# Kernel optimization log

Hardware: AMD Instinct MI355X
Metric: run time of the kernel (lower is better)

Reference implementation:

```python
import jax, jax.numpy as jnp
import numpy as np

N_NODES = 100000
N_EDGES = 1000000

def _gcn_conv(x, W, b, src, dst, n_nodes):
    # PyG GCNConv: linear first, then symmetric-normalized aggregation with self loops
    x = x @ W  # [N, F_out]
    loop = jnp.arange(n_nodes, dtype=src.dtype)
    src2 = jnp.concatenate([src, loop])
    dst2 = jnp.concatenate([dst, loop])
    deg = jax.ops.segment_sum(jnp.ones(src2.shape[0], x.dtype), dst2, num_segments=n_nodes)
    dinv = jnp.where(deg > 0, jax.lax.rsqrt(deg), 0.0)
    norm = dinv[src2] * dinv[dst2]  # [E+N]
    msgs = x[src2] * norm[:, None]  # gather + scale
    out = jax.ops.segment_sum(msgs, dst2, num_segments=n_nodes)  # scatter-add
    return out + b

def _pair_norm_si(x):
    # mode 'PN-SI', scale=1
    x = x - x.mean(axis=0)
    row_norm = jnp.sqrt(1e-6 + jnp.sum(x * x, axis=1, keepdims=True))
    return x / row_norm

def setup_inputs() -> dict:
    key = jax.random.key(0)
    k1, k2, k3, k4 = jax.random.split(key, 4)
    in_c, hid_c, out_c = 256, 64, 40
    x = jax.random.normal(k1, (N_NODES, in_c), dtype=jnp.float32)
    edge_index = jax.random.randint(k2, (2, N_EDGES), 0, N_NODES, dtype=jnp.int64)
    W1 = jax.random.normal(k3, (in_c, hid_c), dtype=jnp.float32) / np.sqrt(in_c)
    b1 = jnp.zeros((hid_c,), jnp.float32)
    W2 = jax.random.normal(k4, (hid_c, out_c), dtype=jnp.float32) / np.sqrt(hid_c)
    b2 = jnp.zeros((out_c,), jnp.float32)
    return {"x": x, "edge_index": edge_index, "W1": W1, "b1": b1, "W2": W2, "b2": b2}

def reference(x, edge_index, W1, b1, W2, b2):
    src, dst = edge_index[0], edge_index[1]
    n = x.shape[0]
    h = jax.nn.relu(_gcn_conv(x, W1, b1, src, dst, n))
    h = _gcn_conv(h, W2, b2, src, dst, n)
    h = _pair_norm_si(h)
    return jax.nn.log_softmax(h, axis=1)
```

## Files before the change

### kernel.cpp

```cpp
#include <hip/hip_runtime.h>
#include <hip/hip_fp16.h>
#include <math.h>

#define F_IN  256
#define F_HID 64
#define F_OUT 40
#define HS2_LD 64

__global__ void k_deg(const int* __restrict__ dst, unsigned* __restrict__ degc, int E) {
    int i = blockIdx.x * blockDim.x + threadIdx.x;
    if (i < E) atomicAdd(&degc[dst[i]], 1u);
}

__global__ __launch_bounds__(256) void k_scanA(const unsigned* __restrict__ degc,
                                               unsigned* __restrict__ exscan,
                                               unsigned* __restrict__ bsum, int N) {
    __shared__ unsigned s[256];
    int tid = threadIdx.x;
    int i = blockIdx.x * 256 + tid;
    unsigned v = (i < N) ? degc[i] : 0u;
    s[tid] = v;
    __syncthreads();
    for (int off = 1; off < 256; off <<= 1) {
        unsigned t = (tid >= off) ? s[tid - off] : 0u;
        __syncthreads();
        s[tid] += t;
        __syncthreads();
    }
    if (i < N) exscan[i] = s[tid] - v;
    if (tid == 255) bsum[blockIdx.x] = s[255];
}

__global__ __launch_bounds__(512) void k_scanB(unsigned* __restrict__ bsum, int nb) {
    __shared__ unsigned s[512];
    int tid = threadIdx.x;
    unsigned v = (tid < nb) ? bsum[tid] : 0u;
    s[tid] = v;
    __syncthreads();
    for (int off = 1; off < 512; off <<= 1) {
        unsigned t = (tid >= off) ? s[tid - off] : 0u;
        __syncthreads();
        s[tid] += t;
        __syncthreads();
    }
    if (tid < nb) bsum[tid] = s[tid] - v;
}

__global__ void k_scanC(const unsigned* __restrict__ degc, const unsigned* __restrict__ exscan,
                        const unsigned* __restrict__ bsum, unsigned* __restrict__ rowptr,
                        float* __restrict__ dinv, int N, int E) {
    int i = blockIdx.x * blockDim.x + threadIdx.x;
    if (i < N) {
        rowptr[i] = exscan[i] + bsum[i >> 8];
        dinv[i] = rsqrtf((float)degc[i] + 1.0f);
        if (i == 0) rowptr[N] = (unsigned)E;
    }
}

__global__ void k_fill(const int* __restrict__ src, const int* __restrict__ dst,
                       const unsigned* __restrict__ rowptr, unsigned* __restrict__ cursor,
                       unsigned* __restrict__ col, int E) {
    int e = blockIdx.x * blockDim.x + threadIdx.x;
    if (e >= E) return;
    int d = dst[e];
    unsigned p = atomicAdd(&cursor[d], 1u);
    col[rowptr[d] + p] = (unsigned)src[e];
}

#define MM1_KC 32
#define MM1_XP 68
__global__ __launch_bounds__(256) void k_mm1(const float* __restrict__ x,
                                             const float* __restrict__ W1,
                                             const float* __restrict__ dinv,
                                             __half* __restrict__ hs1, int N) {
    __shared__ float sX[MM1_KC][MM1_XP];
    __shared__ float sW[MM1_KC][F_HID];
    int tid = threadIdx.x;
    int nbase = blockIdx.x * 64;
    int n0 = (tid & 15) * 4;
    int f0 = (tid >> 4) * 4;

    float acc[4][4];
    #pragma unroll
    for (int i = 0; i < 4; ++i)
        #pragma unroll
        for (int j = 0; j < 4; ++j) acc[i][j] = 0.f;

    for (int k0 = 0; k0 < F_IN; k0 += MM1_KC) {
        #pragma unroll
        for (int q = tid; q < 512; q += 256) {
            int row = q >> 3;
            int c4  = q & 7;
            int node = nbase + row;
            float4 v = (node < N) ? *(const float4*)(x + (size_t)node * F_IN + k0 + c4 * 4)
                                  : make_float4(0.f, 0.f, 0.f, 0.f);
            sX[c4 * 4 + 0][row] = v.x;
            sX[c4 * 4 + 1][row] = v.y;
            sX[c4 * 4 + 2][row] = v.z;
            sX[c4 * 4 + 3][row] = v.w;
        }
        #pragma unroll
        for (int q = tid; q < 512; q += 256) {
            int r  = q >> 4;
            int c4 = q & 15;
            *(float4*)&sW[r][c4 * 4] = *(const float4*)(W1 + (size_t)(k0 + r) * F_HID + c4 * 4);
        }
        __syncthreads();

        #pragma unroll
        for (int k = 0; k < MM1_KC; ++k) {
            float4 xv = *(const float4*)&sX[k][n0];
            float4 wv = *(const float4*)&sW[k][f0];
            acc[0][0] = fmaf(xv.x, wv.x, acc[0][0]); acc[0][1] = fmaf(xv.x, wv.y, acc[0][1]);
            acc[0][2] = fmaf(xv.x, wv.z, acc[0][2]); acc[0][3] = fmaf(xv.x, wv.w, acc[0][3]);
            acc[1][0] = fmaf(xv.y, wv.x, acc[1][0]); acc[1][1] = fmaf(xv.y, wv.y, acc[1][1]);
            acc[1][2] = fmaf(xv.y, wv.z, acc[1][2]); acc[1][3] = fmaf(xv.y, wv.w, acc[1][3]);
            acc[2][0] = fmaf(xv.z, wv.x, acc[2][0]); acc[2][1] = fmaf(xv.z, wv.y, acc[2][1]);
            acc[2][2] = fmaf(xv.z, wv.z, acc[2][2]); acc[2][3] = fmaf(xv.z, wv.w, acc[2][3]);
            acc[3][0] = fmaf(xv.w, wv.x, acc[3][0]); acc[3][1] = fmaf(xv.w, wv.y, acc[3][1]);
            acc[3][2] = fmaf(xv.w, wv.z, acc[3][2]); acc[3][3] = fmaf(xv.w, wv.w, acc[3][3]);
        }
        __syncthreads();
    }

    #pragma unroll
    for (int i = 0; i < 4; ++i) {
        int node = nbase + n0 + i;
        if (node < N) {
            float din = dinv[node];
            __half2* p = (__half2*)(hs1 + (size_t)node * F_HID + f0);
            p[0] = __floats2half2_rn(acc[i][0] * din, acc[i][1] * din);
            p[1] = __floats2half2_rn(acc[i][2] * din, acc[i][3] * din);
        }
    }
}

__global__ __launch_bounds__(256) void k_agg1(const unsigned* __restrict__ rowptr,
                                              const unsigned* __restrict__ col,
                                              const float* __restrict__ dinv,
                                              const __half* __restrict__ hs1,
                                              const float* __restrict__ bias1,
                                              float* __restrict__ agg1, int N) {
    int lane = threadIdx.x & 63;
    int w = blockIdx.x * 4 + (threadIdx.x >> 6);
    int na = 2 * w, nb = 2 * w + 1;
    if (na >= N) return;

    float dinA = dinv[na];
    unsigned aE = rowptr[na], aEnd = rowptr[na + 1];
    float accA = __half2float(hs1[(size_t)na * F_HID + lane]);

    bool hasB = (nb < N);
    float dinB = 0.f, accB = 0.f;
    unsigned bE = 0, bEnd = 0;
    if (hasB) {
        dinB = dinv[nb];
        bE = rowptr[nb]; bEnd = rowptr[nb + 1];
        accB = __half2float(hs1[(size_t)nb * F_HID + lane]);
    }

    while (aE + 4 <= aEnd && bE + 4 <= bEnd) {
        unsigned sa0 = col[aE], sa1 = col[aE + 1], sa2 = col[aE + 2], sa3 = col[aE + 3];
        unsigned sb0 = col[bE], sb1 = col[bE + 1], sb2 = col[bE + 2], sb3 = col[bE + 3];
        float va0 = __half2float(hs1[(size_t)sa0 * F_HID + lane]);
        float va1 = __half2float(hs1[(size_t)sa1 * F_HID + lane]);
        float va2 = __half2float(hs1[(size_t)sa2 * F_HID + lane]);
        float va3 = __half2float(hs1[(size_t)sa3 * F_HID + lane]);
        float vb0 = __half2float(hs1[(size_t)sb0 * F_HID + lane]);
        float vb1 = __half2float(hs1[(size_t)sb1 * F_HID + lane]);
        float vb2 = __half2float(hs1[(size_t)sb2 * F_HID + lane]);
        float vb3 = __half2float(hs1[(size_t)sb3 * F_HID + lane]);
        accA += (va0 + va1) + (va2 + va3);
        accB += (vb0 + vb1) + (vb2 + vb3);
        aE += 4; bE += 4;
    }
    while (aE + 4 <= aEnd) {
        unsigned s0 = col[aE], s1 = col[aE + 1], s2 = col[aE + 2], s3 = col[aE + 3];
        float v0 = __half2float(hs1[(size_t)s0 * F_HID + lane]);
        float v1 = __half2float(hs1[(size_t)s1 * F_HID + lane]);
        float v2 = __half2float(hs1[(size_t)s2 * F_HID + lane]);
        float v3 = __half2float(hs1[(size_t)s3 * F_HID + lane]);
        accA += (v0 + v1) + (v2 + v3);
        aE += 4;
    }
    while (bE + 4 <= bEnd) {
        unsigned s0 = col[bE], s1 = col[bE + 1], s2 = col[bE + 2], s3 = col[bE + 3];
        float v0 = __half2float(hs1[(size_t)s0 * F_HID + lane]);
        float v1 = __half2float(hs1[(size_t)s1 * F_HID + lane]);
        float v2 = __half2float(hs1[(size_t)s2 * F_HID + lane]);
        float v3 = __half2float(hs1[(size_t)s3 * F_HID + lane]);
        accB += (v0 + v1) + (v2 + v3);
        bE += 4;
    }
    while (aE < aEnd && bE < bEnd) {
        unsigned sa = col[aE], sb = col[bE];
        accA += __half2float(hs1[(size_t)sa * F_HID + lane]);
        accB += __half2float(hs1[(size_t)sb * F_HID + lane]);
        ++aE; ++bE;
    }
    while (aE < aEnd) { accA += __half2float(hs1[(size_t)col[aE] * F_HID + lane]); ++aE; }
    while (bE < bEnd) { accB += __half2float(hs1[(size_t)col[bE] * F_HID + lane]); ++bE; }

    float bv = bias1[lane];
    float vA = accA * dinA + bv;
    agg1[(size_t)na * F_HID + lane] = vA > 0.f ? vA : 0.f;
    if (hasB) {
        float vB = accB * dinB + bv;
        agg1[(size_t)nb * F_HID + lane] = vB > 0.f ? vB : 0.f;
    }
}

__global__ __launch_bounds__(320) void k_mm2(const float* __restrict__ a,
                                             const float* __restrict__ W2,
                                             const float* __restrict__ dinv,
                                             __half* __restrict__ hs2, int N) {
    __shared__ float sW[F_HID * F_OUT];
    int tid = threadIdx.x;
    for (int idx = tid; idx < F_HID * F_OUT; idx += 320) sW[idx] = W2[idx];
    __syncthreads();

    int f = tid % F_OUT, r = tid / F_OUT;
    int node = blockIdx.x * 8 + r;
    if (node >= N) return;
    const float* ar = a + (size_t)node * F_HID;
    float acc = 0.f;
    #pragma unroll 8
    for (int k = 0; k < F_HID; ++k) acc = fmaf(ar[k], sW[k * F_OUT + f], acc);
    hs2[(size_t)node * HS2_LD + f] = __float2half(acc * dinv[node]);
}

__global__ __launch_bounds__(256) void k_agg2(const unsigned* __restrict__ rowptr,
                                              const unsigned* __restrict__ col,
                                              const float* __restrict__ dinv,
                                              const __half* __restrict__ hs2,
                                              float* __restrict__ out,
                                              float* __restrict__ colsum, int N) {
    __shared__ float part[256];
    int lane = threadIdx.x & 63;
    int wid = threadIdx.x >> 6;
    int nwaves = gridDim.x * 4;
    float cacc = 0.f;
    if (lane < F_OUT) {
        for (int w = blockIdx.x * 4 + wid; 2 * w < N; w += nwaves) {
            int na = 2 * w, nb = 2 * w + 1;
            float dinA = dinv[na];
            unsigned aE = rowptr[na], aEnd = rowptr[na + 1];
            float accA = __half2float(hs2[(size_t)na * HS2_LD + lane]);
            bool hasB = (nb < N);
            float dinB = 0.f, accB = 0.f;
            unsigned bE = 0, bEnd = 0;
            if (hasB) {
                dinB = dinv[nb];
                bE = rowptr[nb]; bEnd = rowptr[nb + 1];
                accB = __half2float(hs2[(size_t)nb * HS2_LD + lane]);
            }

            while (aE + 4 <= aEnd && bE + 4 <= bEnd) {
                unsigned sa0 = col[aE], sa1 = col[aE + 1], sa2 = col[aE + 2], sa3 = col[aE + 3];
                unsigned sb0 = col[bE], sb1 = col[bE + 1], sb2 = col[bE + 2], sb3 = col[bE + 3];
                float va0 = __half2float(hs2[(size_t)sa0 * HS2_LD + lane]);
                float va1 = __half2float(hs2[(size_t)sa1 * HS2_LD + lane]);
                float va2 = __half2float(hs2[(size_t)sa2 * HS2_LD + lane]);
                float va3 = __half2float(hs2[(size_t)sa3 * HS2_LD + lane]);
                float vb0 = __half2float(hs2[(size_t)sb0 * HS2_LD + lane]);
                float vb1 = __half2float(hs2[(size_t)sb1 * HS2_LD + lane]);
                float vb2 = __half2float(hs2[(size_t)sb2 * HS2_LD + lane]);
                float vb3 = __half2float(hs2[(size_t)sb3 * HS2_LD + lane]);
                accA += (va0 + va1) + (va2 + va3);
                accB += (vb0 + vb1) + (vb2 + vb3);
                aE += 4; bE += 4;
            }
            while (aE + 4 <= aEnd) {
                unsigned s0 = col[aE], s1 = col[aE + 1], s2 = col[aE + 2], s3 = col[aE + 3];
                float v0 = __half2float(hs2[(size_t)s0 * HS2_LD + lane]);
                float v1 = __half2float(hs2[(size_t)s1 * HS2_LD + lane]);
                float v2 = __half2float(hs2[(size_t)s2 * HS2_LD + lane]);
                float v3 = __half2float(hs2[(size_t)s3 * HS2_LD + lane]);
                accA += (v0 + v1) + (v2 + v3);
                aE += 4;
            }
            while (bE + 4 <= bEnd) {
                unsigned s0 = col[bE], s1 = col[bE + 1], s2 = col[bE + 2], s3 = col[bE + 3];
                float v0 = __half2float(hs2[(size_t)s0 * HS2_LD + lane]);
                float v1 = __half2float(hs2[(size_t)s1 * HS2_LD + lane]);
                float v2 = __half2float(hs2[(size_t)s2 * HS2_LD + lane]);
                float v3 = __half2float(hs2[(size_t)s3 * HS2_LD + lane]);
                accB += (v0 + v1) + (v2 + v3);
                bE += 4;
            }
            while (aE < aEnd && bE < bEnd) {
                unsigned sa = col[aE], sb = col[bE];
                accA += __half2float(hs2[(size_t)sa * HS2_LD + lane]);
                accB += __half2float(hs2[(size_t)sb * HS2_LD + lane]);
                ++aE; ++bE;
            }
            while (aE < aEnd) { accA += __half2float(hs2[(size_t)col[aE] * HS2_LD + lane]); ++aE; }
            while (bE < bEnd) { accB += __half2float(hs2[(size_t)col[bE] * HS2_LD + lane]); ++bE; }

            accA *= dinA;
            out[(size_t)na * F_OUT + lane] = accA;
            cacc += accA;
            if (hasB) {
                accB *= dinB;
                out[(size_t)nb * F_OUT + lane] = accB;
                cacc += accB;
            }
        }
    }
    part[threadIdx.x] = cacc;
    __syncthreads();
    if (threadIdx.x < F_OUT) {
        float s = part[threadIdx.x] + part[64 + threadIdx.x] + part[128 + threadIdx.x] + part[192 + threadIdx.x];
        atomicAdd(&colsum[threadIdx.x], s);
    }
}

__global__ __launch_bounds__(128) void k_final(float* __restrict__ out,
                                               const float* __restrict__ colsum, int N) {
    __shared__ float sMean[F_OUT];
    if (threadIdx.x < F_OUT) sMean[threadIdx.x] = colsum[threadIdx.x] * (1.0f / (float)N);
    __syncthreads();
    int n = blockIdx.x * blockDim.x + threadIdx.x;
    if (n >= N) return;
    float* row = out + (size_t)n * F_OUT;
    float v[F_OUT];
    float ss = 0.f;
    #pragma unroll
    for (int f = 0; f < F_OUT; ++f) {
        float t = row[f] - sMean[f];
        v[f] = t;
        ss += t * t;
    }
    float scale = 1.0f / sqrtf(ss + 1e-6f);
    float m = -1e30f;
    #pragma unroll
    for (int f = 0; f < F_OUT; ++f) {
        float y = v[f] * scale;
        v[f] = y;
        m = fmaxf(m, y);
    }
    float sum = 0.f;
    #pragma unroll
    for (int f = 0; f < F_OUT; ++f) sum += expf(v[f] - m);
    float lse = logf(sum);
    #pragma unroll
    for (int f = 0; f < F_OUT; ++f) row[f] = v[f] - m - lse;
}

extern "C" void kernel_launch(void* const* d_in, const int* in_sizes, int n_in,
                              void* d_out, int out_size, void* d_ws, size_t ws_size,
                              hipStream_t stream) {
    const float* x  = (const float*)d_in[0];
    const int*   ei = (const int*)d_in[1];
    const float* W1 = (const float*)d_in[2];
    const float* b1 = (const float*)d_in[3];
    const float* W2 = (const float*)d_in[4];
    float* out = (float*)d_out;

    int N = in_sizes[0] / F_IN;
    int E = in_sizes[1] / 2;
    const int* src = ei;
    const int* dst = ei + E;

    unsigned* degc   = (unsigned*)d_ws;
    unsigned* cursor = degc + N;
    float*    colsum = (float*)(cursor + N);
    unsigned* rowptr = (unsigned*)(colsum + 64);
    unsigned* col    = rowptr + N + 1;
    float*    dinv   = (float*)(col + E);
    float*    agg1   = dinv + N;
    __half*   hs1    = (__half*)(agg1 + (size_t)64 * N);
    __half*   hs2    = hs1 + (size_t)64 * N;
    unsigned* exscan = (unsigned*)agg1;
    unsigned* bsum   = exscan + N;

    hipMemsetAsync(d_ws, 0, ((size_t)2 * N + 64) * sizeof(float), stream);

    int nA = (N + 255) / 256;
    k_deg<<<(E + 255) / 256, 256, 0, stream>>>(dst, degc, E);
    k_scanA<<<nA, 256, 0, stream>>>(degc, exscan, bsum, N);
    k_scanB<<<1, 512, 0, stream>>>(bsum, nA);
    k_scanC<<<nA, 256, 0, stream>>>(degc, exscan, bsum, rowptr, dinv, N, E);
    k_fill<<<(E + 255) / 256, 256, 0, stream>>>(src, dst, rowptr, cursor, col, E);
    k_mm1<<<(N + 63) / 64, 256, 0, stream>>>(x, W1, dinv, hs1, N);
    int waves1 = (N + 1) / 2;
    k_agg1<<<(waves1 + 3) / 4, 256, 0, stream>>>(rowptr, col, dinv, hs1, b1, agg1, N);
    k_mm2<<<(N + 7) / 8, 320, 0, stream>>>(agg1, W2, dinv, hs2, N);
    k_agg2<<<2048, 256, 0, stream>>>(rowptr, col, dinv, hs2, out, colsum, N);
    k_final<<<(N + 127) / 128, 128, 0, stream>>>(out, colsum, N);
}
```

Baseline: 448.6 us.

## Use fp16 MFMA for first-layer matmul with pre-transposed fp16 weights

Replaces the scalar FP32 FMA tiling in the first linear layer with 16x16x32 fp16 MFMA instructions. A small new kernel first converts W1 to a transposed fp16 copy, and each wave keeps its slice of that copy in registers. x tiles are converted to fp16 in shared memory, cutting compute time for the 100k x 256 x 64 matmul. The cost is fp16 rounding of the inputs, an extra kernel launch, and 2-byte scattered output stores in place of half2 stores.

```diff
diff --git a/kernel.cpp b/kernel.cpp
--- a/kernel.cpp
+++ b/kernel.cpp
@@ -6,6 +6,10 @@
 #define F_HID 64
 #define F_OUT 40
 #define HS2_LD 64
+
+typedef _Float16 h8 __attribute__((ext_vector_type(8)));
+typedef _Float16 h4 __attribute__((ext_vector_type(4)));
+typedef float f4 __attribute__((ext_vector_type(4)));
 
 __global__ void k_deg(const int* __restrict__ dst, unsigned* __restrict__ degc, int E) {
     int i = blockIdx.x * blockDim.x + threadIdx.x;
@@ -67,70 +71,70 @@
     col[rowptr[d] + p] = (unsigned)src[e];
 }
 
-#define MM1_KC 32
-#define MM1_XP 68
+__global__ void k_wt(const float* __restrict__ W1, __half* __restrict__ Wt) {
+    int i = blockIdx.x * 256 + threadIdx.x;
+    int k = i >> 6, n = i & 63;
+    Wt[n * 256 + k] = __float2half(W1[i]);
+}
+
+#define XS 136
 __global__ __launch_bounds__(256) void k_mm1(const float* __restrict__ x,
-                                             const float* __restrict__ W1,
+                                             const __half* __restrict__ Wth,
                                              const float* __restrict__ dinv,
-                                             __half* __restrict__ hs1, int N) {
-    __shared__ float sX[MM1_KC][MM1_XP];
-    __shared__ float sW[MM1_KC][F_HID];
+                                             __half* __restrict__ hs1o, int N) {
+    __shared__ _Float16 sX[64 * XS];
+    const _Float16* Wt = (const _Float16*)Wth;
+    _Float16* hs1 = (_Float16*)hs1o;
     int tid = threadIdx.x;
+    int lane = tid & 63;
+    int wv = tid >> 6;
+    int m15 = lane & 15;
+    int q = lane >> 4;
     int nbase = blockIdx.x * 64;
-    int n0 = (tid & 15) * 4;
-    int f0 = (tid >> 4) * 4;
-
-    float acc[4][4];
-    #pragma unroll
-    for (int i = 0; i < 4; ++i)
+
+    h8 bf[8];
+    #pragma unroll
+    for (int kt = 0; kt < 8; ++kt)
+        bf[kt] = *(const h8*)(Wt + (wv * 16 + m15) * 256 + kt * 32 + q * 8);
+
+    f4 acc[4];
+    #pragma unroll
+    for (int mt = 0; mt < 4; ++mt) acc[mt] = (f4){0.f, 0.f, 0.f, 0.f};
+
+    #pragma unroll
+    for (int c = 0; c < 2; ++c) {
         #pragma unroll
-        for (int j = 0; j < 4; ++j) acc[i][j] = 0.f;
-
-    for (int k0 = 0; k0 < F_IN; k0 += MM1_KC) {
+        for (int p = 0; p < 8; ++p) {
+            int idx = p * 256 + tid;
+            int row = idx >> 5;
+            int c4  = idx & 31;
+            int node = nbase + row;
+            float4 v = (node < N) ? *(const float4*)(x + (size_t)node * F_IN + c * 128 + c4 * 4)
+                                  : make_float4(0.f, 0.f, 0.f, 0.f);
+            h4 hv = { (_Float16)v.x, (_Float16)v.y, (_Float16)v.z, (_Float16)v.w };
+            *(h4*)&sX[row * XS + c4 * 4] = hv;
+        }
+        __syncthreads();
         #pragma unroll
-        for (int q = tid; q < 512; q += 256) {
-            int row = q >> 3;
-            int c4  = q & 7;
-            int node = nbase + row;
-            float4 v = (node < N) ? *(const float4*)(x + (size_t)node * F_IN + k0 + c4 * 4)
-                                  : make_float4(0.f, 0.f, 0.f, 0.f);
-            sX[c4 * 4 + 0][row] = v.x;
-            sX[c4 * 4 + 1][row] = v.y;
-            sX[c4 * 4 + 2][row] = v.z;
-            sX[c4 * 4 + 3][row] = v.w;
+        for (int kt2 = 0; kt2 < 4; ++kt2) {
+            #pragma unroll
+            for (int mt = 0; mt < 4; ++mt) {
+                h8 a = *(const h8*)&sX[(mt * 16 + m15) * XS + kt2 * 32 + q * 8];
+                acc[mt] = __builtin_amdgcn_mfma_f32_16x16x32_f16(a, bf[c * 4 + kt2], acc[mt], 0, 0, 0);
+            }
         }
+        __syncthreads();
+    }
+
+    #pragma unroll
+    for (int mt = 0; mt < 4; ++mt) {
         #pragma unroll
-        for (int q = tid; q < 512; q += 256) {
-            int r  = q >> 4;
-            int c4 = q & 15;
-            *(float4*)&sW[r][c4 * 4] = *(const float4*)(W1 + (size_t)(k0 + r) * F_HID + c4 * 4);
-        }
-        __syncthreads();
-
-        #pragma unroll
-        for (int k = 0; k < MM1_KC; ++k) {
-            float4 xv = *(const float4*)&sX[k][n0];
-            float4 wv = *(const float4*)&sW[k][f0];
-            acc[0][0] = fmaf(xv.x, wv.x, acc[0][0]); acc[0][1] = fmaf(xv.x, wv.y, acc[0][1]);
-            acc[0][2] = fmaf(xv.x, wv.z, acc[0][2]); acc[0][3] = fmaf(xv.x, wv.w, acc[0][3]);
-            acc[1][0] = fmaf(xv.y, wv.x, acc[1][0]); acc[1][1] = fmaf(xv.y, wv.y, acc[1][1]);
-            acc[1][2] = fmaf(xv.y, wv.z, acc[1][2]); acc[1][3] = fmaf(xv.y, wv.w, acc[1][3]);
-            acc[2][0] = fmaf(xv.z, wv.x, acc[2][0]); acc[2][1] = fmaf(xv.z, wv.y, acc[2][1]);
-            acc[2][2] = fmaf(xv.z, wv.z, acc[2][2]); acc[2][3] = fmaf(xv.z, wv.w, acc[2][3]);
-            acc[3][0] = fmaf(xv.w, wv.x, acc[3][0]); acc[3][1] = fmaf(xv.w, wv.y, acc[3][1]);
-            acc[3][2] = fmaf(xv.w, wv.z, acc[3][2]); acc[3][3] = fmaf(xv.w, wv.w, acc[3][3]);
-        }
-        __syncthreads();
-    }
-
-    #pragma unroll
-    for (int i = 0; i < 4; ++i) {
-        int node = nbase + n0 + i;
-        if (node < N) {
-            float din = dinv[node];
-            __half2* p = (__half2*)(hs1 + (size_t)node * F_HID + f0);
-            p[0] = __floats2half2_rn(acc[i][0] * din, acc[i][1] * din);
-            p[1] = __floats2half2_rn(acc[i][2] * din, acc[i][3] * din);
+        for (int r = 0; r < 4; ++r) {
+            int node = nbase + mt * 16 + q * 4 + r;
+            if (node < N) {
+                float din = dinv[node];
+                hs1[(size_t)node * F_HID + wv * 16 + m15] = (_Float16)(acc[mt][r] * din);
+            }
         }
     }
 }
@@ -371,6 +375,7 @@
     float*    agg1   = dinv + N;
     __half*   hs1    = (__half*)(agg1 + (size_t)64 * N);
     __half*   hs2    = hs1 + (size_t)64 * N;
+    __half*   Wt     = hs2 + (size_t)64 * N;
     unsigned* exscan = (unsigned*)agg1;
     unsigned* bsum   = exscan + N;
 
@@ -382,7 +387,8 @@
     k_scanB<<<1, 512, 0, stream>>>(bsum, nA);
     k_scanC<<<nA, 256, 0, stream>>>(degc, exscan, bsum, rowptr, dinv, N, E);
     k_fill<<<(E + 255) / 256, 256, 0, stream>>>(src, dst, rowptr, cursor, col, E);
-    k_mm1<<<(N + 63) / 64, 256, 0, stream>>>(x, W1, dinv, hs1, N);
+    k_wt<<<64, 256, 0, stream>>>(W1, Wt);
+    k_mm1<<<(N + 63) / 64, 256, 0, stream>>>(x, Wt, dinv, hs1, N);
     int waves1 = (N + 1) / 2;
     k_agg1<<<(waves1 + 3) / 4, 256, 0, stream>>>(rowptr, col, dinv, hs1, b1, agg1, N);
     k_mm2<<<(N + 7) / 8, 320, 0, stream>>>(agg1, W2, dinv, hs2, N);
```

Measured after the change: 443.5 us. Within noise of the previous version (-1.1%).
